# Kernel optimization log

Measured on AMD Instinct MI355X. Metric: run time of the kernel, lower is better.

The kernel has to match this reference:

```python
import jax, jax.numpy as jnp
import numpy as np

B, S, E, H = 2, 2048, 2048, 16
D = E // H  # head_dim = 128
EPS = 1e-5


def setup_inputs() -> dict:
    key = jax.random.key(0)
    ks = jax.random.split(key, 16)
    s_e = 1.0 / np.sqrt(E)
    s_f = 1.0 / np.sqrt(4 * E)
    return {
        "x": jax.random.normal(ks[0], (B, S, E), jnp.float32),
        "ln1_w": jnp.ones((E,), jnp.float32) + 0.01 * jax.random.normal(ks[1], (E,)),
        "ln1_b": 0.01 * jax.random.normal(ks[2], (E,)),
        "wq": s_e * jax.random.normal(ks[3], (E, E), jnp.float32),
        "wk": s_e * jax.random.normal(ks[4], (E, E), jnp.float32),
        "wv": s_e * jax.random.normal(ks[5], (E, E), jnp.float32),
        "wo": s_e * jax.random.normal(ks[6], (E, E), jnp.float32),
        "bo": 0.01 * jax.random.normal(ks[7], (E,)),
        "ln2_w": jnp.ones((E,), jnp.float32) + 0.01 * jax.random.normal(ks[8], (E,)),
        "ln2_b": 0.01 * jax.random.normal(ks[9], (E,)),
        "w1": s_e * jax.random.normal(ks[10], (E, 4 * E), jnp.float32),
        "b1": 0.01 * jax.random.normal(ks[11], (4 * E,)),
        "w2": s_f * jax.random.normal(ks[12], (4 * E, E), jnp.float32),
        "b2": 0.01 * jax.random.normal(ks[13], (E,)),
    }


def _layernorm(x, w, b):
    mu = jnp.mean(x, axis=-1, keepdims=True)
    var = jnp.var(x, axis=-1, keepdims=True)
    return (x - mu) * jax.lax.rsqrt(var + EPS) * w + b


def _attention(x, wq, wk, wv, wo, bo):
    # x: [B,S,E] -> q,k,v: [B,H,S,D]
    def split(t):
        return t.reshape(B, S, H, D).transpose(0, 2, 1, 3)
    q = split(x @ wq)
    k = split(x @ wk)
    v = split(x @ wv)
    scores = jnp.einsum("bhqd,bhkd->bhqk", q, k)  # [B,H,S,S]
    causal = jnp.triu(jnp.ones((S, S), bool), k=1)
    scores = jnp.where(causal, -jnp.inf, scores)
    # NOTE: faithful to source -- scaling applied after masking, inside softmax arg
    attn = jax.nn.softmax(scores / np.sqrt(D), axis=-1)
    ctx = jnp.einsum("bhqk,bhkd->bhqd", attn, v)
    ctx = ctx.transpose(0, 2, 1, 3).reshape(B, S, E)
    return ctx @ wo + bo


def reference(x, ln1_w, ln1_b, wq, wk, wv, wo, bo, ln2_w, ln2_b, w1, b1, w2, b2):
    shortcut = x
    x1 = _layernorm(x, ln1_w, ln1_b)
    attn_out = _attention(x1, wq, wk, wv, wo, bo)
    a = attn_out + shortcut
    # NOTE: faithful to source quirk -- second shortcut is post-LN1 x1, not a
    y = _layernorm(a, ln2_w, ln2_b)
    y = jax.nn.gelu(y @ w1 + b1, approximate=False) @ w2 + b2
    return x1 + y
```

## Files before the change

### kernel.cpp

```cpp
#include <hip/hip_runtime.h>
#include <math.h>

typedef unsigned short u16;
typedef unsigned int u32;
typedef __attribute__((ext_vector_type(8))) short short8;
typedef __attribute__((ext_vector_type(4))) float f32x4;
typedef __attribute__((ext_vector_type(16))) float f32x16;
typedef __attribute__((ext_vector_type(4))) u32 u32x4;
typedef __attribute__((ext_vector_type(2))) u32 u32x2;

#define DEVFN static __device__ __forceinline__

DEVFN u16 f2bf(float x) {
  union { float f; u32 u; } v; v.f = x;
  u32 r = v.u + 0x7fffu + ((v.u >> 16) & 1u);
  return (u16)(r >> 16);
}
DEVFN float bf2f(u16 h) {
  union { u32 u; float f; } v; v.u = ((u32)h) << 16;
  return v.f;
}
DEVFN u32 packbf2(float a, float b) {
  return (u32)f2bf(a) | ((u32)f2bf(b) << 16);
}
DEVFN void gl2lds16(const u16* g, u16* l) {
  __builtin_amdgcn_global_load_lds(
      (const __attribute__((address_space(1))) u32*)g,
      (__attribute__((address_space(3))) u32*)l, 16, 0, 0);
}
DEVFN float gelu_exact(float v) {
  float s = v * 0.70710678118654752f;
  float ax = fabsf(s);
  float t = __builtin_amdgcn_rcpf(1.0f + 0.3275911f * ax);
  float poly = t * (0.254829592f +
               t * (-0.284496736f +
               t * (1.421413741f +
               t * (-1.453152027f + t * 1.061405429f))));
  float e = __expf(-s * s);
  float er = 1.0f - poly * e;
  er = (s < 0.f) ? -er : er;
  return 0.5f * v * (1.0f + er);
}

#define VMW8() asm volatile("s_waitcnt vmcnt(8)" ::: "memory")
#define VMW6() asm volatile("s_waitcnt vmcnt(6)" ::: "memory")
#define VMW0() asm volatile("s_waitcnt vmcnt(0)" ::: "memory")
#define LGKM0() asm volatile("s_waitcnt lgkmcnt(0)" ::: "memory")
#define CFENCE() asm volatile("" ::: "memory")
#define BARRIER() do { CFENCE(); __builtin_amdgcn_s_barrier(); CFENCE(); } while (0)
#define SCHED0() __builtin_amdgcn_sched_barrier(0)

__global__ __launch_bounds__(256) void tconvall_k(
    const float* __restrict__ wq, const float* __restrict__ wk,
    const float* __restrict__ wv, const float* __restrict__ wo,
    const float* __restrict__ w1, const float* __restrict__ w2,
    u16* __restrict__ wqt, u16* __restrict__ wkt, u16* __restrict__ wvt,
    u16* __restrict__ wot, u16* __restrict__ w1t, u16* __restrict__ w2t) {
  __shared__ float tile[32][33];
  int b = blockIdx.x;
  const float* in; u16* out; int K, N, tn, tk;
  if (b < 16384) {
    int wsel = b >> 12;
    int loc = b & 4095;
    in = (wsel == 0) ? wq : (wsel == 1) ? wk : (wsel == 2) ? wv : wo;
    out = (wsel == 0) ? wqt : (wsel == 1) ? wkt : (wsel == 2) ? wvt : wot;
    K = 2048; N = 2048; tn = loc & 63; tk = loc >> 6;
  } else if (b < 32768) {
    int loc = b - 16384; in = w1; out = w1t; K = 2048; N = 8192;
    tn = loc & 255; tk = loc >> 8;
  } else {
    int loc = b - 32768; in = w2; out = w2t; K = 8192; N = 2048;
    tn = loc & 63; tk = loc >> 6;
  }
  int n0 = tn << 5, k0 = tk << 5;
  int tx = threadIdx.x & 31, ty = threadIdx.x >> 5;
#pragma unroll
  for (int i = 0; i < 32; i += 8)
    tile[ty + i][tx] = in[(long)(k0 + ty + i) * N + n0 + tx];
  __syncthreads();
#pragma unroll
  for (int i = 0; i < 32; i += 8)
    out[(long)(n0 + ty + i) * K + k0 + tx] = f2bf(tile[tx][ty + i]);
}

__global__ __launch_bounds__(256) void ln1_k(const float* __restrict__ x,
                                             const float* __restrict__ w,
                                             const float* __restrict__ b,
                                             float* __restrict__ y32,
                                             u16* __restrict__ y16) {
  long base = (long)blockIdx.x * 2048;
  int t = threadIdx.x;
  float4 v0 = ((const float4*)(x + base))[2 * t];
  float4 v1 = ((const float4*)(x + base))[2 * t + 1];
  float xv[8];
  *(float4*)xv = v0; *(float4*)(xv + 4) = v1;
  float s = 0.f, ss = 0.f;
#pragma unroll
  for (int i = 0; i < 8; ++i) { s += xv[i]; ss += xv[i] * xv[i]; }
#pragma unroll
  for (int m = 1; m < 64; m <<= 1) { s += __shfl_xor(s, m); ss += __shfl_xor(ss, m); }
  __shared__ float rs[4], rss[4];
  int wave = t >> 6;
  if ((t & 63) == 0) { rs[wave] = s; rss[wave] = ss; }
  __syncthreads();
  s = rs[0] + rs[1] + rs[2] + rs[3];
  ss = rss[0] + rss[1] + rss[2] + rss[3];
  float mean = s * (1.f / 2048.f);
  float var = ss * (1.f / 2048.f) - mean * mean;
  float inv = rsqrtf(var + 1e-5f);
  float wv[8], bv[8];
  *(float4*)wv = ((const float4*)w)[2 * t]; *(float4*)(wv + 4) = ((const float4*)w)[2 * t + 1];
  *(float4*)bv = ((const float4*)b)[2 * t]; *(float4*)(bv + 4) = ((const float4*)b)[2 * t + 1];
  float yv[8];
#pragma unroll
  for (int i = 0; i < 8; ++i) yv[i] = (xv[i] - mean) * inv * wv[i] + bv[i];
  ((float4*)(y32 + base))[2 * t] = *(float4*)yv;
  ((float4*)(y32 + base))[2 * t + 1] = *(float4*)(yv + 4);
  u32x4 ov;
#pragma unroll
  for (int i = 0; i < 4; ++i) ov[i] = packbf2(yv[2 * i], yv[2 * i + 1]);
  ((u32x4*)(y16 + base))[t] = ov;
}

__global__ __launch_bounds__(256) void ln2_k(const u16* __restrict__ a,
                                             const float* __restrict__ w,
                                             const float* __restrict__ b,
                                             u16* __restrict__ y) {
  long base = (long)blockIdx.x * 2048;
  int t = threadIdx.x;
  u32x4 pv = ((const u32x4*)(a + base))[t];
  float xv[8];
#pragma unroll
  for (int i = 0; i < 4; ++i) {
    xv[2 * i] = bf2f((u16)(pv[i] & 0xffffu));
    xv[2 * i + 1] = bf2f((u16)(pv[i] >> 16));
  }
  float s = 0.f, ss = 0.f;
#pragma unroll
  for (int i = 0; i < 8; ++i) { s += xv[i]; ss += xv[i] * xv[i]; }
#pragma unroll
  for (int m = 1; m < 64; m <<= 1) { s += __shfl_xor(s, m); ss += __shfl_xor(ss, m); }
  __shared__ float rs[4], rss[4];
  int wave = t >> 6;
  if ((t & 63) == 0) { rs[wave] = s; rss[wave] = ss; }
  __syncthreads();
  s = rs[0] + rs[1] + rs[2] + rs[3];
  ss = rss[0] + rss[1] + rss[2] + rss[3];
  float mean = s * (1.f / 2048.f);
  float var = ss * (1.f / 2048.f) - mean * mean;
  float inv = rsqrtf(var + 1e-5f);
  float wv[8], bv[8];
  *(float4*)wv = ((const float4*)w)[2 * t]; *(float4*)(wv + 4) = ((const float4*)w)[2 * t + 1];
  *(float4*)bv = ((const float4*)b)[2 * t]; *(float4*)(bv + 4) = ((const float4*)b)[2 * t + 1];
  u32x4 ov;
#pragma unroll
  for (int i = 0; i < 4; ++i) {
    float y0 = (xv[2 * i] - mean) * inv * wv[2 * i] + bv[2 * i];
    float y1 = (xv[2 * i + 1] - mean) * inv * wv[2 * i + 1] + bv[2 * i + 1];
    ov[i] = packbf2(y0, y1);
  }
  ((u32x4*)(y + base))[t] = ov;
}

template <int MODE>
__global__ __launch_bounds__(512, 1) void gemm8p_k(const u16* __restrict__ A,
                                                   const u16* __restrict__ W,
                                                   void* __restrict__ outp,
                                                   const float* __restrict__ bias) {
  constexpr int nM = 16;
  constexpr int nN = (MODE == 0) ? 24 : (MODE == 3) ? 32 : 8;
  constexpr int KS = (MODE == 5) ? 2 : 1;
  constexpr int KK = (MODE == 5) ? 4096 : 2048;
  constexpr long LD = (MODE == 5) ? 8192 : 2048;
  constexpr int nt = KK / 64;
  constexpr int nwg = nM * nN * KS;
  __shared__ __align__(16) u16 lds[2][32768];
  const int t = threadIdx.x, lane = t & 63, wave = t >> 6;
  const int g = lane >> 4, r16 = lane & 15;
  const int wm = wave >> 2, wn = wave & 3;
  const int orig = blockIdx.y * gridDim.x + blockIdx.x;
  const int sw = (orig & 7) * (nwg >> 3) + (orig >> 3);
  const int mi = sw % nM;
  const int rest = sw / nM;
  const int ni = (MODE == 5) ? (rest & 7) : rest;
  const int ks = (MODE == 5) ? (rest >> 3) : 0;
  const long m0 = (long)mi * 256, n0 = (long)ni * 256;
  const long k0 = (long)ks * 4096;
  const int rl = lane >> 3, cl = lane & 7;

  auto stAq = [&](int b, int grp, int ts) {
#pragma unroll
    for (int q = 0; q < 2; ++q) {
      int rb = q * 128 + grp * 64 + wave * 8;
      int rr = rb + rl;
      gl2lds16(A + (m0 + rr) * LD + k0 + (long)ts * 64 + (cl ^ (rr & 7)) * 8,
               &lds[b][rb * 64]);
    }
  };
  auto stBq = [&](int b, int grp, int ts) {
#pragma unroll
    for (int q = 0; q < 2; ++q) {
      int rb = q * 128 + (wave >> 2) * 64 + (wave & 3) * 8 + grp * 32;
      int rr = rb + rl;
      gl2lds16(W + (n0 + rr) * LD + k0 + (long)ts * 64 + (cl ^ (rr & 7)) * 8,
               &lds[b][16384 + rb * 64]);
    }
  };

  f32x4 acc[8][4] = {};
  short8 afl[4][2], afh[4][2], bfl[2][2], bfh[2][2];

  stAq(0, 0, 0); stBq(0, 0, 0); stAq(0, 1, 0); stBq(0, 1, 0);
  stAq(1, 0, 1); stBq(1, 0, 1); stAq(1, 1, 1); stBq(1, 1, 1);
  VMW8();
  BARRIER();

  for (int tt = 0; tt < nt; ++tt) {
    const int cur = tt & 1;
    const u16* Lc = &lds[cur][0];
    const int ts = (tt + 2 < nt) ? tt + 2 : nt - 1;
#pragma unroll
    for (int ii = 0; ii < 4; ++ii) {
      int row = wm * 128 + ii * 16 + r16;
#pragma unroll
      for (int kk = 0; kk < 2; ++kk)
        afl[ii][kk] = *(const short8*)(Lc + row * 64 + (((kk << 2) | g) ^ (row & 7)) * 8);
    }
#pragma unroll
    for (int jj = 0; jj < 2; ++jj) {
      int row = wn * 64 + jj * 16 + r16;
#pragma unroll
      for (int kk = 0; kk < 2; ++kk)
        bfl[jj][kk] = *(const short8*)(Lc + 16384 + row * 64 + (((kk << 2) | g) ^ (row & 7)) * 8);
    }
    BARRIER(); LGKM0(); SCHED0();
    __builtin_amdgcn_s_setprio(1);
#pragma unroll
    for (int ii = 0; ii < 4; ++ii)
#pragma unroll
      for (int jj = 0; jj < 2; ++jj)
#pragma unroll
        for (int kk = 0; kk < 2; ++kk)
          acc[ii][jj] = __builtin_amdgcn_mfma_f32_16x16x32_bf16(
              afl[ii][kk], bfl[jj][kk], acc[ii][jj], 0, 0, 0);
    __builtin_amdgcn_s_setprio(0);
    SCHED0();
    BARRIER();
#pragma unroll
    for (int jj = 0; jj < 2; ++jj) {
      int row = wn * 64 + 32 + jj * 16 + r16;
#pragma unroll
      for (int kk = 0; kk < 2; ++kk)
        bfh[jj][kk] = *(const short8*)(Lc + 16384 + row * 64 + (((kk << 2) | g) ^ (row & 7)) * 8);
    }
    stAq(cur, 0, ts);
    BARRIER(); LGKM0(); SCHED0();
    __builtin_amdgcn_s_setprio(1);
#pragma unroll
    for (int ii = 0; ii < 4; ++ii)
#pragma unroll
      for (int jj = 0; jj < 2; ++jj)
#pragma unroll
        for (int kk = 0; kk < 2; ++kk)
          acc[ii][2 + jj] = __builtin_amdgcn_mfma_f32_16x16x32_bf16(
              afl[ii][kk], bfh[jj][kk], acc[ii][2 + jj], 0, 0, 0);
    __builtin_amdgcn_s_setprio(0);
    SCHED0();
    BARRIER();
#pragma unroll
    for (int ii = 0; ii < 4; ++ii) {
      int row = wm * 128 + 64 + ii * 16 + r16;
#pragma unroll
      for (int kk = 0; kk < 2; ++kk)
        afh[ii][kk] = *(const short8*)(Lc + row * 64 + (((kk << 2) | g) ^ (row & 7)) * 8);
    }
    stBq(cur, 0, ts);
    BARRIER(); LGKM0(); SCHED0();
    __builtin_amdgcn_s_setprio(1);
#pragma unroll
    for (int ii = 0; ii < 4; ++ii)
#pragma unroll
      for (int jj = 0; jj < 2; ++jj)
#pragma unroll
        for (int kk = 0; kk < 2; ++kk)
          acc[4 + ii][jj] = __builtin_amdgcn_mfma_f32_16x16x32_bf16(
              afh[ii][kk], bfl[jj][kk], acc[4 + ii][jj], 0, 0, 0);
    __builtin_amdgcn_s_setprio(0);
    SCHED0();
    BARRIER();
    stAq(cur, 1, ts); stBq(cur, 1, ts);
    SCHED0();
    __builtin_amdgcn_s_setprio(1);
#pragma unroll
    for (int ii = 0; ii < 4; ++ii)
#pragma unroll
      for (int jj = 0; jj < 2; ++jj)
#pragma unroll
        for (int kk = 0; kk < 2; ++kk)
          acc[4 + ii][2 + jj] = __builtin_amdgcn_mfma_f32_16x16x32_bf16(
              afh[ii][kk], bfh[jj][kk], acc[4 + ii][2 + jj], 0, 0, 0);
    __builtin_amdgcn_s_setprio(0);
    SCHED0();
    VMW6();
    BARRIER();
  }
  VMW0();

#pragma unroll
  for (int ii = 0; ii < 8; ++ii) {
#pragma unroll
    for (int jj = 0; jj < 4; ++jj) {
#pragma unroll
      for (int r = 0; r < 4; ++r) {
        long mg = m0 + wm * 128 + ii * 16 + g * 4 + r;
        long ng = n0 + wn * 64 + jj * 16 + r16;
        float v = acc[ii][jj][r];
        if constexpr (MODE == 0) {
          long which = ng >> 11;
          long nloc = ng & 2047;
          long bb = mg >> 11, sq = mg & 2047;
          long hh = nloc >> 7, dd = nloc & 127;
          long idx = (which < 2) ? (((bb * 16 + hh) * 2048 + sq) * 128 + dd)
                                 : (((bb * 16 + hh) * 128 + dd) * 2048 + sq);
          ((u16*)outp)[which * 8388608 + idx] = f2bf(v);
        } else if constexpr (MODE == 3) {
          v = gelu_exact(v + bias[ng]);
          ((u16*)outp)[mg * 8192 + ng] = f2bf(v);
        } else {
          ((float*)outp)[(long)ks * 8388608 + mg * 2048 + ng] = v;
        }
      }
    }
  }
}

__global__ __launch_bounds__(256) void red_k(const float* __restrict__ p,
                                             const float* __restrict__ bias,
                                             const float* __restrict__ resid,
                                             float* __restrict__ out) {
  long i = (long)blockIdx.x * 256 + threadIdx.x;
  for (long idx = i; idx < 2097152; idx += 2048 * 256) {
    float4 a = ((const float4*)p)[idx];
    float4 b = ((const float4*)(p + 8388608))[idx];
    float4 r = ((const float4*)resid)[idx];
    float4 bs = ((const float4*)bias)[idx & 511];
    float4 o;
    o.x = a.x + b.x + r.x + bs.x;
    o.y = a.y + b.y + r.y + bs.y;
    o.z = a.z + b.z + r.z + bs.z;
    o.w = a.w + b.w + r.w + bs.w;
    ((float4*)out)[idx] = o;
  }
}

template <int MODE>
__global__ __launch_bounds__(512, 2) void gemm3_k(const u16* __restrict__ A,
                                                  const u16* __restrict__ W,
                                                  void* __restrict__ outp,
                                                  const float* __restrict__ bias,
                                                  const float* __restrict__ resid,
                                                  int M, int N, int K) {
  __shared__ __align__(16) u16 lds[3][24576];
  const int t = threadIdx.x, lane = t & 63, wave = t >> 6;
  const int g = lane >> 4, r16 = lane & 15;
  const int wm = wave >> 2, wn = wave & 3;
  const int nM = M >> 7;
  const int nwg = gridDim.x * gridDim.y;
  const int orig = blockIdx.y * gridDim.x + blockIdx.x;
  const int sw = (nwg & 7) ? orig : ((orig & 7) * (nwg >> 3) + (orig >> 3));
  const long m0 = (long)(sw % nM) * 128, n0 = (long)(sw / nM) * 256;
  const int nt = K >> 6;
  const long Kl = K;
  const int rl = lane >> 3, cc = lane & 7;

  auto stA = [&](u16* Lb, long tile) {
#pragma unroll
    for (int q = 0; q < 2; ++q) {
      int rr = (wave * 2 + q) * 8 + rl;
      int c = cc ^ (rr & 7);
      gl2lds16(A + (m0 + rr) * Kl + (tile << 6) + c * 8, Lb + (wave * 2 + q) * 512);
    }
  };
  auto stB = [&](u16* Lb, int half, long tile) {
#pragma unroll
    for (int q = 0; q < 2; ++q) {
      int rr = (wave * 2 + q) * 8 + rl;
      int c = cc ^ (rr & 7);
      gl2lds16(W + (n0 + half * 128 + rr) * Kl + (tile << 6) + c * 8,
               Lb + 8192 + half * 8192 + (wave * 2 + q) * 512);
    }
  };

  f32x4 acc[4][4] = {};
  u16* L0 = &lds[0][0];
  u16* L1 = &lds[1][0];
  u16* L2 = &lds[2][0];

  stA(L0, 0); stB(L0, 0, 0); stB(L0, 1, 0);
  if (nt > 1) { stA(L1, 1); stB(L1, 0, 1); stB(L1, 1, 1); }
  if (nt > 2) { VMW6(); } else { VMW0(); }
  BARRIER();

  for (int tt = 0; tt < nt; ++tt) {
    const long ts = (tt + 2 < nt) ? (long)(tt + 2) : (long)(nt - 1);
    short8 af[4][2], bf[2][2];
#pragma unroll
    for (int ii2 = 0; ii2 < 4; ++ii2) {
      int row = (ii2 * 2 + wm) * 16 + r16;
#pragma unroll
      for (int kk = 0; kk < 2; ++kk)
        af[ii2][kk] = *(const short8*)(L0 + row * 64 + (((kk << 2) | g) ^ (row & 7)) * 8);
    }
#pragma unroll
    for (int jj2 = 0; jj2 < 2; ++jj2) {
      int row = (jj2 * 4 + wn) * 16 + r16;
#pragma unroll
      for (int kk = 0; kk < 2; ++kk)
        bf[jj2][kk] = *(const short8*)(L0 + 8192 + row * 64 + (((kk << 2) | g) ^ (row & 7)) * 8);
    }
    stA(L2, ts); stB(L2, 0, ts);
    __builtin_amdgcn_s_setprio(1);
#pragma unroll
    for (int ii2 = 0; ii2 < 4; ++ii2)
#pragma unroll
      for (int jj2 = 0; jj2 < 2; ++jj2)
#pragma unroll
        for (int kk = 0; kk < 2; ++kk)
          acc[ii2][jj2] = __builtin_amdgcn_mfma_f32_16x16x32_bf16(
              af[ii2][kk], bf[jj2][kk], acc[ii2][jj2], 0, 0, 0);
    __builtin_amdgcn_s_setprio(0);
    BARRIER();
#pragma unroll
    for (int jj2 = 0; jj2 < 2; ++jj2) {
      int row = ((2 + jj2) * 4 + wn) * 16 + r16;
#pragma unroll
      for (int kk = 0; kk < 2; ++kk)
        bf[jj2][kk] = *(const short8*)(L0 + 8192 + row * 64 + (((kk << 2) | g) ^ (row & 7)) * 8);
    }
    stB(L2, 1, ts);
    __builtin_amdgcn_s_setprio(1);
#pragma unroll
    for (int ii2 = 0; ii2 < 4; ++ii2)
#pragma unroll
      for (int jj2 = 0; jj2 < 2; ++jj2)
#pragma unroll
        for (int kk = 0; kk < 2; ++kk)
          acc[ii2][2 + jj2] = __builtin_amdgcn_mfma_f32_16x16x32_bf16(
              af[ii2][kk], bf[jj2][kk], acc[ii2][2 + jj2], 0, 0, 0);
    __builtin_amdgcn_s_setprio(0);
    VMW6(); BARRIER();
    u16* tmp = L0; L0 = L1; L1 = L2; L2 = tmp;
  }
  VMW0();

  const long Nl = N;
#pragma unroll
  for (int ii = 0; ii < 4; ++ii) {
#pragma unroll
    for (int jj = 0; jj < 4; ++jj) {
#pragma unroll
      for (int r = 0; r < 4; ++r) {
        long mg = m0 + (ii * 2 + wm) * 16 + g * 4 + r;
        long ng = n0 + (jj * 4 + wn) * 16 + r16;
        float v = acc[ii][jj][r];
        v += bias[ng] + resid[mg * Nl + ng];
        if constexpr (MODE == 2) {
          ((u16*)outp)[mg * Nl + ng] = f2bf(v);
        } else {
          ((float*)outp)[mg * Nl + ng] = v;
        }
      }
    }
  }
}

__global__ __launch_bounds__(256, 2) void attn2_k(const u16* __restrict__ Qp,
                                                  const u16* __restrict__ Kp,
                                                  const u16* __restrict__ Vp,
                                                  u16* __restrict__ ctx) {
  __shared__ __align__(16) u16 KsL[2][64 * 128];
  __shared__ __align__(16) u16 VsL[2][128 * 64];
  const int qt = gridDim.x - 1 - blockIdx.x;
  const int bh = blockIdx.y;
  const int t = threadIdx.x, lane = t & 63, wave = t >> 6;
  const int l31 = lane & 31, hi = lane >> 5;
  const int q0 = qt * 128, qw0 = q0 + wave * 32;
  const int qg = qw0 + l31;
  const u16* Qh = Qp + (long)bh * 2048 * 128;
  const u16* Kh = Kp + (long)bh * 2048 * 128;
  const u16* Vh = Vp + (long)bh * 128 * 2048;
  const int nkt = qt * 2 + 2;
  const int ktmax = (qw0 + 31) >> 6;
  const float cs = 0.12753042923810058f;

  short8 qf[8];
#pragma unroll
  for (int ds = 0; ds < 8; ++ds)
    qf[ds] = *(const short8*)(Qh + (long)qg * 128 + ds * 16 + hi * 8);

  f32x16 O0 = {}, O1 = {}, O2 = {}, O3 = {};
  float m = -INFINITY, l = 0.f;

  auto stage = [&](int b, int kt) {
#pragma unroll
    for (int q = 0; q < 4; ++q) {
      int r = wave * 16 + q * 4 + (lane >> 4);
      int c = (lane & 15) ^ (r & 15);
      gl2lds16(Kh + ((long)kt * 64 + r) * 128 + c * 8,
               &KsL[b][(wave * 16 + q * 4) * 128]);
    }
#pragma unroll
    for (int q = 0; q < 4; ++q) {
      int r = wave * 32 + q * 8 + (lane >> 3);
      int c = (lane & 7) ^ (r & 7);
      gl2lds16(Vh + (long)r * 2048 + kt * 64 + c * 8,
               &VsL[b][(wave * 32 + q * 8) * 64]);
    }
  };

  stage(0, 0);
  VMW0(); BARRIER();

  for (int kt = 0; kt < nkt; ++kt) {
    const int cur = kt & 1;
    if (kt + 1 < nkt) stage(cur ^ 1, kt + 1);
    if (kt <= ktmax) {
      f32x16 S0 = {}, S1 = {};
      __builtin_amdgcn_s_setprio(1);
#pragma unroll
      for (int ds = 0; ds < 8; ++ds) {
        int c0 = ((ds * 2 + hi) ^ (l31 & 15)) * 8;
        short8 k0 = *(const short8*)(&KsL[cur][l31 * 128 + c0]);
        int r1 = 32 + l31;
        int c1 = ((ds * 2 + hi) ^ (r1 & 15)) * 8;
        short8 k1 = *(const short8*)(&KsL[cur][r1 * 128 + c1]);
        S0 = __builtin_amdgcn_mfma_f32_32x32x16_bf16(k0, qf[ds], S0, 0, 0, 0);
        S1 = __builtin_amdgcn_mfma_f32_32x32x16_bf16(k1, qf[ds], S1, 0, 0, 0);
      }
      __builtin_amdgcn_s_setprio(0);
      float p[32];
#pragma unroll
      for (int i = 0; i < 16; ++i) { p[i] = S0[i]; p[16 + i] = S1[i]; }
      if (kt * 64 + 63 > qw0) {
#pragma unroll
        for (int ks = 0; ks < 2; ++ks)
#pragma unroll
          for (int r = 0; r < 16; ++r) {
            int kg = kt * 64 + ks * 32 + (r & 3) + 8 * (r >> 2) + 4 * hi;
            if (kg > qg) p[ks * 16 + r] = -INFINITY;
          }
      }
      float tmax = p[0];
#pragma unroll
      for (int i = 1; i < 32; ++i) tmax = fmaxf(tmax, p[i]);
      tmax = fmaxf(tmax, __shfl_xor(tmax, 32));
      float mnew = fmaxf(m, tmax);
      float corr = __builtin_amdgcn_exp2f((m - mnew) * cs);
      float ls = 0.f;
#pragma unroll
      for (int i = 0; i < 32; ++i) {
        p[i] = __builtin_amdgcn_exp2f((p[i] - mnew) * cs);
        ls += p[i];
      }
      ls += __shfl_xor(ls, 32);
      l = l * corr + ls;
      m = mnew;
#pragma unroll
      for (int i = 0; i < 16; ++i) {
        O0[i] *= corr; O1[i] *= corr; O2[i] *= corr; O3[i] *= corr;
      }
      short8 pf[4];
#pragma unroll
      for (int gg = 0; gg < 4; ++gg) {
        u32 u_, v_, w_, z_;
        asm("v_cvt_pk_bf16_f32 %0, %1, %2" : "=v"(u_) : "v"(p[gg * 8 + 0]), "v"(p[gg * 8 + 1]));
        asm("v_cvt_pk_bf16_f32 %0, %1, %2" : "=v"(v_) : "v"(p[gg * 8 + 2]), "v"(p[gg * 8 + 3]));
        asm("v_cvt_pk_bf16_f32 %0, %1, %2" : "=v"(w_) : "v"(p[gg * 8 + 4]), "v"(p[gg * 8 + 5]));
        asm("v_cvt_pk_bf16_f32 %0, %1, %2" : "=v"(z_) : "v"(p[gg * 8 + 6]), "v"(p[gg * 8 + 7]));
        asm("v_permlane32_swap_b32 %0, %1" : "+v"(u_), "+v"(w_));
        asm("v_permlane32_swap_b32 %0, %1" : "+v"(v_), "+v"(z_));
        union { u32 w4[4]; short8 s; } cv;
        cv.w4[0] = u_; cv.w4[1] = v_; cv.w4[2] = w_; cv.w4[3] = z_;
        pf[gg] = cv.s;
      }
      __builtin_amdgcn_s_setprio(1);
#define PVROW(ds, OO)                                                          \
  {                                                                            \
    int row = (ds)*32 + l31;                                                   \
    _Pragma("unroll") for (int gg = 0; gg < 4; ++gg) {                         \
      short8 vf = *(const short8*)(&VsL[cur][row * 64 +                        \
                                             (((gg * 2 + hi) ^ (row & 7)) * 8)]); \
      OO = __builtin_amdgcn_mfma_f32_32x32x16_bf16(vf, pf[gg], OO, 0, 0, 0);   \
    }                                                                          \
  }
      PVROW(0, O0); PVROW(1, O1); PVROW(2, O2); PVROW(3, O3);
#undef PVROW
      __builtin_amdgcn_s_setprio(0);
    }
    VMW0(); BARRIER();
  }

  const float inv = 1.f / l;
  u16* cp = ctx + ((long)(bh >> 4) * 2048 + qg) * 2048 + (bh & 15) * 128;
#define WROUT(OO, dsb)                                                         \
  _Pragma("unroll") for (int rg = 0; rg < 4; ++rg) {                           \
    int d = (dsb)*32 + 8 * rg + 4 * hi;                                        \
    u32x2 wv;                                                                  \
    wv[0] = packbf2(OO[4 * rg] * inv, OO[4 * rg + 1] * inv);                   \
    wv[1] = packbf2(OO[4 * rg + 2] * inv, OO[4 * rg + 3] * inv);               \
    *(u32x2*)(cp + d) = wv;                                                    \
  }
  WROUT(O0, 0); WROUT(O1, 1); WROUT(O2, 2); WROUT(O3, 3);
#undef WROUT
}

extern "C" void kernel_launch(void* const* d_in, const int* in_sizes, int n_in,
                              void* d_out, int out_size, void* d_ws, size_t ws_size,
                              hipStream_t stream) {
  const float* x = (const float*)d_in[0];
  const float* ln1w = (const float*)d_in[1];
  const float* ln1b = (const float*)d_in[2];
  const float* wq = (const float*)d_in[3];
  const float* wk = (const float*)d_in[4];
  const float* wv = (const float*)d_in[5];
  const float* wo = (const float*)d_in[6];
  const float* bo = (const float*)d_in[7];
  const float* ln2w = (const float*)d_in[8];
  const float* ln2b = (const float*)d_in[9];
  const float* w1 = (const float*)d_in[10];
  const float* b1 = (const float*)d_in[11];
  const float* w2 = (const float*)d_in[12];
  const float* b2 = (const float*)d_in[13];
  float* out = (float*)d_out;
  char* ws = (char*)d_ws;

  float* x1f = (float*)(ws + 0);
  u16* x1b = (u16*)(ws + 33554432);
  u16* wqt = (u16*)(ws + 50331648);
  u16* wkt = (u16*)(ws + 58720256);
  u16* wvt = (u16*)(ws + 67108864);
  u16* wot = (u16*)(ws + 75497472);
  u16* w1t = (u16*)(ws + 83886080);
  u16* w2t = (u16*)(ws + 117440512);
  u16* qb = (u16*)(ws + 150994944);
  u16* kb = (u16*)(ws + 167772160);
  u16* vb = (u16*)(ws + 184549376);
  u16* ctxb = (u16*)(ws + 201326592);
  u16* ab = (u16*)(ws + 218103808);
  u16* y0b = (u16*)(ws + 234881024);
  u16* hb = qb;
  float* pbuf = (float*)(ws + 50331648);

  tconvall_k<<<49152, 256, 0, stream>>>(wq, wk, wv, wo, w1, w2,
                                        wqt, wkt, wvt, wot, w1t, w2t);
  ln1_k<<<4096, 256, 0, stream>>>(x, ln1w, ln1b, x1f, x1b);
  gemm8p_k<0><<<dim3(16, 24), 512, 0, stream>>>(x1b, wqt, qb, nullptr);
  attn2_k<<<dim3(16, 32), 256, 0, stream>>>(qb, kb, vb, ctxb);
  gemm3_k<2><<<dim3(32, 8), 512, 0, stream>>>(ctxb, wot, ab, bo, x, 4096, 2048, 2048);
  ln2_k<<<4096, 256, 0, stream>>>(ab, ln2w, ln2b, y0b);
  gemm8p_k<3><<<dim3(16, 32), 512, 0, stream>>>(y0b, w1t, hb, b1);
  gemm8p_k<5><<<dim3(16, 16), 512, 0, stream>>>(hb, w2t, pbuf, nullptr);
  red_k<<<2048, 256, 0, stream>>>(pbuf, b2, x1f, out);
}
```

Before: 631.8 us.

## Prefetch next tile's LDS fragments during MFMA and relax wait counts in GEMM loop

Restructures the 256x256 bf16 GEMM main loop so the A-low and B-low fragments for the next k-tile are read from the other LDS buffer while the current tile's later MFMA quadrants run. Partial lgkmcnt/vmcnt waits replace full drains. The order of the global-to-LDS stage issues is also changed (B group 1 now goes before B group 0). The aim is to hide LDS read latency behind MFMA work and cut stalls at each barrier. The cost is more complex wait-count reasoning, with a risk of races if the counts do not match the outstanding operations.

```diff
diff --git a/kernel.cpp b/kernel.cpp
--- a/kernel.cpp
+++ b/kernel.cpp
@@ -44,8 +44,11 @@
 
 #define VMW8() asm volatile("s_waitcnt vmcnt(8)" ::: "memory")
 #define VMW6() asm volatile("s_waitcnt vmcnt(6)" ::: "memory")
+#define VMW2() asm volatile("s_waitcnt vmcnt(2)" ::: "memory")
 #define VMW0() asm volatile("s_waitcnt vmcnt(0)" ::: "memory")
 #define LGKM0() asm volatile("s_waitcnt lgkmcnt(0)" ::: "memory")
+#define LGKM4() asm volatile("s_waitcnt lgkmcnt(4)" ::: "memory")
+#define LGKM8() asm volatile("s_waitcnt lgkmcnt(8)" ::: "memory")
 #define CFENCE() asm volatile("" ::: "memory")
 #define BARRIER() do { CFENCE(); __builtin_amdgcn_s_barrier(); CFENCE(); } while (0)
 #define SCHED0() __builtin_amdgcn_sched_barrier(0)
@@ -210,101 +213,86 @@
   f32x4 acc[8][4] = {};
   short8 afl[4][2], afh[4][2], bfl[2][2], bfh[2][2];
 
+#define RD_AFL(Lp)                                                            \
+  _Pragma("unroll") for (int ii = 0; ii < 4; ++ii) {                          \
+    int row = wm * 128 + ii * 16 + r16;                                       \
+    _Pragma("unroll") for (int kk = 0; kk < 2; ++kk)                          \
+        afl[ii][kk] = *(const short8*)((Lp) + row * 64 +                      \
+                                       (((kk << 2) | g) ^ (row & 7)) * 8);    \
+  }
+#define RD_AFH(Lp)                                                            \
+  _Pragma("unroll") for (int ii = 0; ii < 4; ++ii) {                          \
+    int row = wm * 128 + 64 + ii * 16 + r16;                                  \
+    _Pragma("unroll") for (int kk = 0; kk < 2; ++kk)                          \
+        afh[ii][kk] = *(const short8*)((Lp) + row * 64 +                      \
+                                       (((kk << 2) | g) ^ (row & 7)) * 8);    \
+  }
+#define RD_BFL(Lp)                                                            \
+  _Pragma("unroll") for (int jj = 0; jj < 2; ++jj) {                          \
+    int row = wn * 64 + jj * 16 + r16;                                        \
+    _Pragma("unroll") for (int kk = 0; kk < 2; ++kk)                          \
+        bfl[jj][kk] = *(const short8*)((Lp) + 16384 + row * 64 +              \
+                                       (((kk << 2) | g) ^ (row & 7)) * 8);    \
+  }
+#define RD_BFH(Lp)                                                            \
+  _Pragma("unroll") for (int jj = 0; jj < 2; ++jj) {                          \
+    int row = wn * 64 + 32 + jj * 16 + r16;                                   \
+    _Pragma("unroll") for (int kk = 0; kk < 2; ++kk)                          \
+        bfh[jj][kk] = *(const short8*)((Lp) + 16384 + row * 64 +              \
+                                       (((kk << 2) | g) ^ (row & 7)) * 8);    \
+  }
+#define MFMA16(AF, BF, I0, J0)                                                \
+  __builtin_amdgcn_s_setprio(1);                                              \
+  _Pragma("unroll") for (int ii = 0; ii < 4; ++ii)                            \
+      _Pragma("unroll") for (int jj = 0; jj < 2; ++jj)                        \
+          _Pragma("unroll") for (int kk = 0; kk < 2; ++kk)                    \
+              acc[(I0) + ii][(J0) + jj] =                                     \
+                  __builtin_amdgcn_mfma_f32_16x16x32_bf16(                    \
+                      AF[ii][kk], BF[jj][kk], acc[(I0) + ii][(J0) + jj],      \
+                      0, 0, 0);                                               \
+  __builtin_amdgcn_s_setprio(0);
+
   stAq(0, 0, 0); stBq(0, 0, 0); stAq(0, 1, 0); stBq(0, 1, 0);
   stAq(1, 0, 1); stBq(1, 0, 1); stAq(1, 1, 1); stBq(1, 1, 1);
   VMW8();
   BARRIER();
+  {
+    const u16* L0p = &lds[0][0];
+    RD_AFL(L0p);
+    RD_BFL(L0p);
+  }
 
   for (int tt = 0; tt < nt; ++tt) {
     const int cur = tt & 1;
     const u16* Lc = &lds[cur][0];
+    const u16* Ln = &lds[cur ^ 1][0];
     const int ts = (tt + 2 < nt) ? tt + 2 : nt - 1;
-#pragma unroll
-    for (int ii = 0; ii < 4; ++ii) {
-      int row = wm * 128 + ii * 16 + r16;
-#pragma unroll
-      for (int kk = 0; kk < 2; ++kk)
-        afl[ii][kk] = *(const short8*)(Lc + row * 64 + (((kk << 2) | g) ^ (row & 7)) * 8);
-    }
-#pragma unroll
-    for (int jj = 0; jj < 2; ++jj) {
-      int row = wn * 64 + jj * 16 + r16;
-#pragma unroll
-      for (int kk = 0; kk < 2; ++kk)
-        bfl[jj][kk] = *(const short8*)(Lc + 16384 + row * 64 + (((kk << 2) | g) ^ (row & 7)) * 8);
-    }
-    BARRIER(); LGKM0(); SCHED0();
-    __builtin_amdgcn_s_setprio(1);
-#pragma unroll
-    for (int ii = 0; ii < 4; ++ii)
-#pragma unroll
-      for (int jj = 0; jj < 2; ++jj)
-#pragma unroll
-        for (int kk = 0; kk < 2; ++kk)
-          acc[ii][jj] = __builtin_amdgcn_mfma_f32_16x16x32_bf16(
-              afl[ii][kk], bfl[jj][kk], acc[ii][jj], 0, 0, 0);
-    __builtin_amdgcn_s_setprio(0);
+    RD_BFH(Lc);
+    BARRIER(); LGKM4(); SCHED0();
+    MFMA16(afl, bfl, 0, 0);
     SCHED0();
     BARRIER();
-#pragma unroll
-    for (int jj = 0; jj < 2; ++jj) {
-      int row = wn * 64 + 32 + jj * 16 + r16;
-#pragma unroll
-      for (int kk = 0; kk < 2; ++kk)
-        bfh[jj][kk] = *(const short8*)(Lc + 16384 + row * 64 + (((kk << 2) | g) ^ (row & 7)) * 8);
-    }
+    RD_AFH(Lc);
     stAq(cur, 0, ts);
-    BARRIER(); LGKM0(); SCHED0();
-    __builtin_amdgcn_s_setprio(1);
-#pragma unroll
-    for (int ii = 0; ii < 4; ++ii)
-#pragma unroll
-      for (int jj = 0; jj < 2; ++jj)
-#pragma unroll
-        for (int kk = 0; kk < 2; ++kk)
-          acc[ii][2 + jj] = __builtin_amdgcn_mfma_f32_16x16x32_bf16(
-              afl[ii][kk], bfh[jj][kk], acc[ii][2 + jj], 0, 0, 0);
-    __builtin_amdgcn_s_setprio(0);
+    VMW2();
+    BARRIER(); LGKM8(); SCHED0();
+    MFMA16(afl, bfh, 0, 2);
     SCHED0();
     BARRIER();
-#pragma unroll
-    for (int ii = 0; ii < 4; ++ii) {
-      int row = wm * 128 + 64 + ii * 16 + r16;
-#pragma unroll
-      for (int kk = 0; kk < 2; ++kk)
-        afh[ii][kk] = *(const short8*)(Lc + row * 64 + (((kk << 2) | g) ^ (row & 7)) * 8);
-    }
-    stBq(cur, 0, ts);
-    BARRIER(); LGKM0(); SCHED0();
-    __builtin_amdgcn_s_setprio(1);
-#pragma unroll
-    for (int ii = 0; ii < 4; ++ii)
-#pragma unroll
-      for (int jj = 0; jj < 2; ++jj)
-#pragma unroll
-        for (int kk = 0; kk < 2; ++kk)
-          acc[4 + ii][jj] = __builtin_amdgcn_mfma_f32_16x16x32_bf16(
-              afh[ii][kk], bfl[jj][kk], acc[4 + ii][jj], 0, 0, 0);
-    __builtin_amdgcn_s_setprio(0);
+    RD_AFL(Ln);
+    stBq(cur, 1, ts);
+    BARRIER(); LGKM8(); SCHED0();
+    MFMA16(afh, bfl, 4, 0);
     SCHED0();
     BARRIER();
-    stAq(cur, 1, ts); stBq(cur, 1, ts);
+    RD_BFL(Ln);
+    stAq(cur, 1, ts); stBq(cur, 0, ts);
+    BARRIER(); SCHED0();
+    MFMA16(afh, bfh, 4, 2);
     SCHED0();
-    __builtin_amdgcn_s_setprio(1);
-#pragma unroll
-    for (int ii = 0; ii < 4; ++ii)
-#pragma unroll
-      for (int jj = 0; jj < 2; ++jj)
-#pragma unroll
-        for (int kk = 0; kk < 2; ++kk)
-          acc[4 + ii][2 + jj] = __builtin_amdgcn_mfma_f32_16x16x32_bf16(
-              afh[ii][kk], bfh[jj][kk], acc[4 + ii][2 + jj], 0, 0, 0);
-    __builtin_amdgcn_s_setprio(0);
-    SCHED0();
-    VMW6();
     BARRIER();
   }
-  VMW0();
+  VMW0(); LGKM0();
 
 #pragma unroll
   for (int ii = 0; ii < 8; ++ii) {
@@ -332,6 +320,11 @@
       }
     }
   }
+#undef RD_AFL
+#undef RD_AFH
+#undef RD_BFL
+#undef RD_BFH
+#undef MFMA16
 }
 
 __global__ __launch_bounds__(256) void red_k(const float* __restrict__ p,
```

Result: slower. 652.9 us (+3.3%).
